# Kernel optimization log

Measured on AMD Instinct MI355X. Metric: run time of the kernel, lower is better.

Reference implementation:

```python
import jax, jax.numpy as jnp
import numpy as np

N_NODES = 100000
N_EDGES = 1600000


def _gcn_layer(feat, W, b, src, dst, n_nodes, pre_transform, activation):
    # GraphConv with norm='right': aggregate copy_src+sum, divide by in-degree (clamped to 1)
    if pre_transform:  # in_feats > out_feats: matmul first, then SpMM
        h = feat @ W
        agg = jax.ops.segment_sum(h[src], dst, num_segments=n_nodes)
    else:              # aggregate first, then matmul
        agg = jax.ops.segment_sum(feat[src], dst, num_segments=n_nodes)
        agg = agg @ W
    deg = jax.ops.segment_sum(jnp.ones((src.shape[0],), feat.dtype), dst, num_segments=n_nodes)
    rst = agg / jnp.clip(deg, 1.0)[:, None]
    rst = rst + b
    if activation:
        rst = jax.nn.relu(rst)
    return rst


def setup_inputs() -> dict:
    key = jax.random.key(0)
    ks = jax.random.split(key, 6)
    def xavier(k, shp):
        bound = float(np.sqrt(6.0 / (shp[0] + shp[1])))
        return jax.random.uniform(k, shp, jnp.float32, -bound, bound)
    return {
        "feat": jax.random.normal(ks[0], (N_NODES, 256), jnp.float32),
        "W0": xavier(ks[1], (256, 64)),
        "b0": jnp.zeros((64,), jnp.float32),
        "W1": xavier(ks[2], (64, 64)),
        "b1": jnp.zeros((64,), jnp.float32),
        "W2": xavier(ks[3], (64, 32)),
        "b2": jnp.zeros((32,), jnp.float32),
        "src": jax.random.randint(ks[4], (N_EDGES,), 0, N_NODES, jnp.int32),
        "dst": jax.random.randint(ks[5], (N_EDGES,), 0, N_NODES, jnp.int32),
    }


def reference(feat, W0, b0, W1, b1, W2, b2, src, dst):
    n = feat.shape[0]
    # layer 0: in 256 > out 64 -> pre-transform; relu
    h = _gcn_layer(feat, W0, b0, src, dst, n, pre_transform=True, activation=True)
    # layer 1: in 64 == out 64 -> aggregate then matmul; relu
    h = _gcn_layer(h, W1, b1, src, dst, n, pre_transform=False, activation=True)
    # layer 2: in 64 > out 32 -> pre-transform; no activation
    h = _gcn_layer(h, W2, b2, src, dst, n, pre_transform=True, activation=False)
    return h
```

## Files before the change

### kernel.cpp

```cpp
#include <hip/hip_runtime.h>
#include <hip/hip_bf16.h>
#include <hip/hip_fp16.h>


constexpr int NB_SHIFT = 7;
constexpr int EPB = 8192;
constexpr int MAXNB = 800;

using half8  = __attribute__((ext_vector_type(8))) _Float16;
using floatx4 = __attribute__((ext_vector_type(4))) float;

__global__ __launch_bounds__(256) void passA_hist(const int* __restrict__ dst, int* __restrict__ C_T,
                                                  int nb, int nblk, int n_edges) {
    __shared__ int h[MAXNB];
    for (int i = threadIdx.x; i < nb; i += 256) h[i] = 0;
    __syncthreads();
    const int e0 = blockIdx.x * EPB;
    const int e1 = min(e0 + EPB, n_edges);
    for (int i = e0 + threadIdx.x; i < e1; i += 256)
        atomicAdd(&h[dst[i] >> NB_SHIFT], 1);
    __syncthreads();
    for (int i = threadIdx.x; i < nb; i += 256)
        C_T[i * nblk + blockIdx.x] = h[i];
}

__global__ __launch_bounds__(256) void bucket_prefix(int* __restrict__ C_T, int* __restrict__ totals,
                                                     int nblk) {
    __shared__ int s[256];
    const int b = blockIdx.x, t = threadIdx.x;
    int v = (t < nblk) ? C_T[b * nblk + t] : 0;
    s[t] = v; __syncthreads();
    for (int off = 1; off < 256; off <<= 1) {
        int x = (t >= off) ? s[t - off] : 0;
        __syncthreads();
        s[t] += x;
        __syncthreads();
    }
    if (t < nblk) C_T[b * nblk + t] = s[t] - v;
    if (t == 255) totals[b] = s[255];
}

__global__ __launch_bounds__(256) void scan_base(const int* __restrict__ totals, int* __restrict__ base_out,
                                                 int* __restrict__ rowptr, int nb, int n, int n_edges) {
    __shared__ int s[256];
    const int t = threadIdx.x;
    int v[4]; int ts = 0;
#pragma unroll
    for (int j = 0; j < 4; ++j) { int i = t * 4 + j; v[j] = (i < nb) ? totals[i] : 0; ts += v[j]; }
    s[t] = ts; __syncthreads();
    for (int off = 1; off < 256; off <<= 1) {
        int x = (t >= off) ? s[t - off] : 0;
        __syncthreads();
        s[t] += x;
        __syncthreads();
    }
    int run = s[t] - ts;
#pragma unroll
    for (int j = 0; j < 4; ++j) { int i = t * 4 + j; if (i < nb) base_out[i] = run; run += v[j]; }
    if (t == 255) base_out[nb] = s[255];
    if (t == 0) rowptr[n] = n_edges;
}

__global__ __launch_bounds__(256) void passB_scatter(const int* __restrict__ src, const int* __restrict__ dst,
                                                     const int* __restrict__ C_T, const int* __restrict__ base,
                                                     int* __restrict__ sorted_pk, int nb, int nblk, int n_edges) {
    __shared__ int cur[MAXNB];
    const int blk = blockIdx.x;
    for (int i = threadIdx.x; i < nb; i += 256) cur[i] = base[i] + C_T[i * nblk + blk];
    __syncthreads();
    const int e0 = blk * EPB;
    const int e1 = min(e0 + EPB, n_edges);
    for (int i = e0 + threadIdx.x; i < e1; i += 256) {
        int d = dst[i];
        int p = atomicAdd(&cur[d >> NB_SHIFT], 1);
        sorted_pk[p] = ((d & 127) << 17) | src[i];
    }
}

__global__ __launch_bounds__(256) void passC_build(const int* __restrict__ sorted_pk, const int* __restrict__ base,
                                                   int* __restrict__ rowptr, int* __restrict__ col,
                                                   float* __restrict__ invd, int n) {
    __shared__ int degl[128];
    __shared__ int s[256];
    __shared__ int curl[128];
    const int b = blockIdx.x, t = threadIdx.x;
    const int node0 = b << NB_SHIFT;
    const int nn = min(128, n - node0);
    const int e0 = base[b], e1 = base[b + 1];
    if (t < 128) degl[t] = 0;
    __syncthreads();
    for (int i = e0 + t; i < e1; i += 256)
        atomicAdd(&degl[sorted_pk[i] >> 17], 1);
    __syncthreads();
    int d = (t < 128) ? degl[t] : 0;
    s[t] = d; __syncthreads();
    for (int off = 1; off < 128; off <<= 1) {
        int x = (t >= off) ? s[t - off] : 0;
        __syncthreads();
        s[t] += x;
        __syncthreads();
    }
    if (t < 128) {
        int excl = s[t] - d;
        curl[t] = excl;
        if (t < nn) {
            rowptr[node0 + t] = e0 + excl;
            invd[node0 + t] = 1.0f / (float)(d > 0 ? d : 1);
        }
    }
    __syncthreads();
    for (int i = e0 + t; i < e1; i += 256) {
        int pk = sorted_pk[i];
        int p = atomicAdd(&curl[pk >> 17], 1);
        col[e0 + p] = pk & 0x1FFFF;
    }
}

__device__ inline float4 load4(const float* p) { return *(const float4*)p; }
__device__ inline float4 load4(const __half* p) {
    __half2 a = *(const __half2*)p;
    __half2 b = *(const __half2*)(p + 2);
    float2 fa = __half22float2(a), fb = __half22float2(b);
    return make_float4(fa.x, fa.y, fb.x, fb.y);
}
__device__ inline void store4(float* p, float x0, float x1, float x2, float x3) {
    *(float4*)p = make_float4(x0, x1, x2, x3);
}
__device__ inline void store4(__half* p, float x0, float x1, float x2, float x3) {
    union { __half h[4]; int2 i2; } u;
    u.h[0] = __float2half(x0); u.h[1] = __float2half(x1);
    u.h[2] = __float2half(x2); u.h[3] = __float2half(x3);
    *(int2*)p = u.i2;
}

template <int FEATS, int EPI, typename OutT>
__global__ __launch_bounds__(256) void agg_kernel(const __half* __restrict__ X, const int* __restrict__ col,
                                                  const int* __restrict__ rowptr,
                                                  const float* __restrict__ inv_deg,
                                                  const float* __restrict__ bias,
                                                  OutT* __restrict__ out, int n) {
    constexpr int LPE = FEATS / 4;
    constexpr int EPW = 64 / LPE;
    const int node = blockIdx.x * 4 + (threadIdx.x >> 6);
    if (node >= n) return;
    const int lane = threadIdx.x & 63;
    const int eg = lane / LPE;
    const int fl = lane % LPE;
    const int s = rowptr[node], e = rowptr[node + 1];

    float ax = 0.f, ay = 0.f, az = 0.f, aw = 0.f;
    if (e > s) {
        int i = s + eg;
        const int nfull = (e - s) / EPW;
        int cc = col[min(i, e - 1)];
#pragma unroll 2
        for (int b = 0; b < nfull; ++b) {
            int cn = col[min(i + EPW, e - 1)];
            const __half* p = X + (size_t)cc * FEATS + fl * 4;
            float2 f01 = __half22float2(*(const __half2*)p);
            float2 f23 = __half22float2(*(const __half2*)(p + 2));
            ax += f01.x; ay += f01.y; az += f23.x; aw += f23.y;
            cc = cn; i += EPW;
        }
        if (i < e) {
            const __half* p = X + (size_t)cc * FEATS + fl * 4;
            float2 f01 = __half22float2(*(const __half2*)p);
            float2 f23 = __half22float2(*(const __half2*)(p + 2));
            ax += f01.x; ay += f01.y; az += f23.x; aw += f23.y;
        }
    }
#pragma unroll
    for (int m = LPE; m < 64; m <<= 1) {
        ax += __shfl_xor(ax, m);
        ay += __shfl_xor(ay, m);
        az += __shfl_xor(az, m);
        aw += __shfl_xor(aw, m);
    }
    if (eg == 0) {
        if (EPI != 0) {
            float sc = inv_deg[node];
            ax = ax * sc + bias[fl * 4 + 0];
            ay = ay * sc + bias[fl * 4 + 1];
            az = az * sc + bias[fl * 4 + 2];
            aw = aw * sc + bias[fl * 4 + 3];
            if (EPI == 1) {
                ax = fmaxf(ax, 0.f); ay = fmaxf(ay, 0.f);
                az = fmaxf(az, 0.f); aw = fmaxf(aw, 0.f);
            }
        }
        store4(&out[(size_t)node * FEATS + fl * 4], ax, ay, az, aw);
    }
}

__global__ __launch_bounds__(256) void cvtW0t(const float* __restrict__ W0, __half* __restrict__ W0t) {
    int o = blockIdx.x * 256 + threadIdx.x;
    int c = o >> 8, k = o & 255;
    W0t[o] = __float2half(W0[k * 64 + c]);
}

__global__ __launch_bounds__(256) void gemm0_mfma(const float* __restrict__ A, const __half* __restrict__ W0t,
                                                  __half* __restrict__ out, int nrows) {
    constexpr int LDH = 280;
    __shared__ _Float16 As[64][LDH];
    __shared__ _Float16 Bs[64][LDH];
    const int t = threadIdx.x;
    const int wave = t >> 6, lane = t & 63;
    const int row0 = blockIdx.x * 64;

#pragma unroll
    for (int l = 0; l < 16; ++l) {
        int fid = t + l * 256;
        int r = fid >> 6, c4 = fid & 63;
        int grow = row0 + r;
        int gr = grow < nrows ? grow : 0;
        float4 v = *(const float4*)&A[(size_t)gr * 256 + c4 * 4];
        _Float16* p = &As[r][c4 * 4];
        p[0] = (_Float16)v.x; p[1] = (_Float16)v.y;
        p[2] = (_Float16)v.z; p[3] = (_Float16)v.w;
    }
#pragma unroll
    for (int l = 0; l < 8; ++l) {
        int fid = t + l * 256;
        int r = fid >> 5, c8 = fid & 31;
        *(half8*)&Bs[r][c8 * 8] = *(const half8*)&W0t[r * 256 + c8 * 8];
    }
    __syncthreads();

    const int ar = wave * 16 + (lane & 15);
    const int kh = (lane >> 4) * 8;
    floatx4 acc0 = {0.f, 0.f, 0.f, 0.f}, acc1 = acc0, acc2 = acc0, acc3 = acc0;
#pragma unroll
    for (int ks = 0; ks < 8; ++ks) {
        const int k0 = ks * 32 + kh;
        half8 a = *(half8*)&As[ar][k0];
        half8 b0 = *(half8*)&Bs[ 0 + (lane & 15)][k0];
        half8 b1 = *(half8*)&Bs[16 + (lane & 15)][k0];
        half8 b2 = *(half8*)&Bs[32 + (lane & 15)][k0];
        half8 b3 = *(half8*)&Bs[48 + (lane & 15)][k0];
        acc0 = __builtin_amdgcn_mfma_f32_16x16x32_f16(a, b0, acc0, 0, 0, 0);
        acc1 = __builtin_amdgcn_mfma_f32_16x16x32_f16(a, b1, acc1, 0, 0, 0);
        acc2 = __builtin_amdgcn_mfma_f32_16x16x32_f16(a, b2, acc2, 0, 0, 0);
        acc3 = __builtin_amdgcn_mfma_f32_16x16x32_f16(a, b3, acc3, 0, 0, 0);
    }

    const int cc = lane & 15;
    const int rb = wave * 16 + (lane >> 4) * 4;
#pragma unroll
    for (int i = 0; i < 4; ++i) {
        int r = row0 + rb + i;
        if (r < nrows) {
            __half* po = &out[(size_t)r * 64];
            po[ 0 + cc] = __float2half(acc0[i]);
            po[16 + cc] = __float2half(acc1[i]);
            po[32 + cc] = __float2half(acc2[i]);
            po[48 + cc] = __float2half(acc3[i]);
        }
    }
}

__global__ __launch_bounds__(256) void gemm12_kernel(const __half* __restrict__ A2, const float* __restrict__ W1,
                                                     const float* __restrict__ b1, const float* __restrict__ W2,
                                                     const float* __restrict__ inv_deg,
                                                     __half* __restrict__ out, int nrows) {
    __shared__ float As[64][68];
    __shared__ float W1s[64][64];
    __shared__ float W2s[64][32];
    const int t = threadIdx.x;
    const int row0 = blockIdx.x * 64;
    const int cg = t % 16, rg = t / 16;

#pragma unroll
    for (int l = 0; l < 4; ++l) {
        int fid = t + l * 256;
        int r = fid / 16, c4 = fid % 16;
        int grow = row0 + r;
        int gr = grow < nrows ? grow : 0;
        float4 v = load4(&A2[(size_t)gr * 64 + c4 * 4]);
        *(float4*)&As[r][c4 * 4] = v;
    }
#pragma unroll
    for (int l = 0; l < 4; ++l) {
        int fid = t + l * 256;
        int r = fid / 16, c4 = fid % 16;
        *(float4*)&W1s[r][c4 * 4] = *(const float4*)&W1[(size_t)r * 64 + c4 * 4];
    }
#pragma unroll
    for (int l = 0; l < 2; ++l) {
        int fid = t + l * 256;
        int r = fid / 8, c4 = fid % 8;
        *(float4*)&W2s[r][c4 * 4] = *(const float4*)&W2[(size_t)r * 32 + c4 * 4];
    }
    __syncthreads();

    float acc[4][4] = {};
#pragma unroll 8
    for (int k = 0; k < 64; ++k) {
        float4 w = *(float4*)&W1s[k][cg * 4];
#pragma unroll
        for (int i = 0; i < 4; ++i) {
            float a = As[rg * 4 + i][k];
            acc[i][0] += a * w.x;
            acc[i][1] += a * w.y;
            acc[i][2] += a * w.z;
            acc[i][3] += a * w.w;
        }
    }
    __syncthreads();

#pragma unroll
    for (int i = 0; i < 4; ++i) {
        int r = row0 + rg * 4 + i;
        float sc = (r < nrows) ? inv_deg[r] : 0.f;
        float x0 = fmaxf(acc[i][0] * sc + b1[cg * 4 + 0], 0.f);
        float x1 = fmaxf(acc[i][1] * sc + b1[cg * 4 + 1], 0.f);
        float x2 = fmaxf(acc[i][2] * sc + b1[cg * 4 + 2], 0.f);
        float x3 = fmaxf(acc[i][3] * sc + b1[cg * 4 + 3], 0.f);
        *(float4*)&As[rg * 4 + i][cg * 4] = make_float4(x0, x1, x2, x3);
    }
    __syncthreads();

    const int cg2 = t % 8, rg2 = t / 8;
    float acc2[2][4] = {};
#pragma unroll 8
    for (int k = 0; k < 64; ++k) {
        float4 w = *(float4*)&W2s[k][cg2 * 4];
#pragma unroll
        for (int i = 0; i < 2; ++i) {
            float a = As[rg2 * 2 + i][k];
            acc2[i][0] += a * w.x;
            acc2[i][1] += a * w.y;
            acc2[i][2] += a * w.z;
            acc2[i][3] += a * w.w;
        }
    }
#pragma unroll
    for (int i = 0; i < 2; ++i) {
        int r = row0 + rg2 * 2 + i;
        if (r < nrows)
            store4(&out[(size_t)r * 32 + cg2 * 4], acc2[i][0], acc2[i][1], acc2[i][2], acc2[i][3]);
    }
}

extern "C" void kernel_launch(void* const* d_in, const int* in_sizes, int n_in,
                              void* d_out, int out_size, void* d_ws, size_t ws_size,
                              hipStream_t stream) {
    const float* feat = (const float*)d_in[0];
    const float* W0   = (const float*)d_in[1];
    const float* b0   = (const float*)d_in[2];
    const float* W1   = (const float*)d_in[3];
    const float* b1   = (const float*)d_in[4];
    const float* W2   = (const float*)d_in[5];
    const float* b2   = (const float*)d_in[6];
    const int*   src  = (const int*)d_in[7];
    const int*   dstv = (const int*)d_in[8];

    const int n = in_sizes[0] / 256;
    const int e = in_sizes[7];

    const int nb   = (n + 127) >> NB_SHIFT;
    const int nblk = (e + EPB - 1) / EPB;

    char* base_p = (char*)d_ws;
    size_t off = 0;
    auto alloc = [&](size_t bytes) -> char* {
        char* p = base_p + off;
        off += (bytes + 255) & ~(size_t)255;
        return p;
    };
    float*  invd   = (float*)alloc((size_t)n * 4);
    int*    rowptr = (int*)alloc((size_t)(n + 1) * 4);
    int*    bbase  = (int*)alloc((size_t)(MAXNB + 1) * 4);
    int*    totals = (int*)alloc((size_t)MAXNB * 4);
    __half* W0t    = (__half*)alloc((size_t)256 * 64 * 2);
    int*    col    = (int*)alloc((size_t)e * 4);
    __half* bufH1  = (__half*)alloc((size_t)n * 64 * 2);
    __half* bufH2  = (__half*)alloc((size_t)n * 64 * 2);
    (void)ws_size;

    int* C_T       = col;
    int* sorted_pk = (int*)bufH1;

    passA_hist   <<<nblk, 256, 0, stream>>>(dstv, C_T, nb, nblk, e);
    bucket_prefix<<<nb,   256, 0, stream>>>(C_T, totals, nblk);
    scan_base    <<<1,    256, 0, stream>>>(totals, bbase, rowptr, nb, n, e);
    passB_scatter<<<nblk, 256, 0, stream>>>(src, dstv, C_T, bbase, sorted_pk, nb, nblk, e);
    passC_build  <<<nb,   256, 0, stream>>>(sorted_pk, bbase, rowptr, col, invd, n);
    cvtW0t       <<<64,   256, 0, stream>>>(W0, W0t);

    const int gemm_blocks = (n + 63) / 64;
    const int agg_blocks  = (n + 3) / 4;

    gemm0_mfma<<<gemm_blocks, 256, 0, stream>>>(feat, W0t, bufH1, n);
    agg_kernel<64, 1, __half><<<agg_blocks, 256, 0, stream>>>(bufH1, col, rowptr, invd, b0, bufH2, n);

    agg_kernel<64, 0, __half><<<agg_blocks, 256, 0, stream>>>(bufH2, col, rowptr, nullptr, nullptr, bufH1, n);
    gemm12_kernel<<<gemm_blocks, 256, 0, stream>>>(bufH1, W1, b1, W2, invd, bufH2, n);

    agg_kernel<32, 2, float><<<agg_blocks, 256, 0, stream>>>(bufH2, col, rowptr, invd, b2, (float*)d_out, n);
}
```

Baseline: 214.8 us.

## Fuse layer-2 matmul into final aggregation and enlarge CSR-build buckets

Layer 2 now aggregates the 64-wide layer-1 output first and applies W2 inside the final aggregation kernel, instead of running the W2 matmul in the gemm kernel and aggregating a 32-wide result. This removes the second matmul stage from the gemm kernel but doubles the gather width of the last SpMM and adds a shared-memory matvec per node. The CSR-build buckets also grow from 128 to 512 nodes, with 512-thread passC blocks, cutting the bucket count and per-bucket overhead.

```diff
diff --git a/kernel.cpp b/kernel.cpp
--- a/kernel.cpp
+++ b/kernel.cpp
@@ -3,11 +3,11 @@
 #include <hip/hip_fp16.h>
 
 
-constexpr int NB_SHIFT = 7;
+constexpr int NB_SHIFT = 9;
 constexpr int EPB = 8192;
-constexpr int MAXNB = 800;
-
-using half8  = __attribute__((ext_vector_type(8))) _Float16;
+constexpr int MAXNB = 200;
+
+using half8   = __attribute__((ext_vector_type(8))) _Float16;
 using floatx4 = __attribute__((ext_vector_type(4))) float;
 
 __global__ __launch_bounds__(256) void passA_hist(const int* __restrict__ dst, int* __restrict__ C_T,
@@ -73,50 +73,47 @@
     for (int i = e0 + threadIdx.x; i < e1; i += 256) {
         int d = dst[i];
         int p = atomicAdd(&cur[d >> NB_SHIFT], 1);
-        sorted_pk[p] = ((d & 127) << 17) | src[i];
-    }
-}
-
-__global__ __launch_bounds__(256) void passC_build(const int* __restrict__ sorted_pk, const int* __restrict__ base,
+        sorted_pk[p] = ((d & 511) << 17) | src[i];
+    }
+}
+
+__global__ __launch_bounds__(512) void passC_build(const int* __restrict__ sorted_pk, const int* __restrict__ base,
                                                    int* __restrict__ rowptr, int* __restrict__ col,
                                                    float* __restrict__ invd, int n) {
-    __shared__ int degl[128];
-    __shared__ int s[256];
-    __shared__ int curl[128];
+    __shared__ int degl[512];
+    __shared__ int s[512];
+    __shared__ int curl[512];
     const int b = blockIdx.x, t = threadIdx.x;
     const int node0 = b << NB_SHIFT;
-    const int nn = min(128, n - node0);
+    const int nn = min(512, n - node0);
     const int e0 = base[b], e1 = base[b + 1];
-    if (t < 128) degl[t] = 0;
-    __syncthreads();
-    for (int i = e0 + t; i < e1; i += 256)
+    degl[t] = 0;
+    __syncthreads();
+    for (int i = e0 + t; i < e1; i += 512)
         atomicAdd(&degl[sorted_pk[i] >> 17], 1);
     __syncthreads();
-    int d = (t < 128) ? degl[t] : 0;
+    int d = degl[t];
     s[t] = d; __syncthreads();
-    for (int off = 1; off < 128; off <<= 1) {
+    for (int off = 1; off < 512; off <<= 1) {
         int x = (t >= off) ? s[t - off] : 0;
         __syncthreads();
         s[t] += x;
         __syncthreads();
     }
-    if (t < 128) {
-        int excl = s[t] - d;
-        curl[t] = excl;
-        if (t < nn) {
-            rowptr[node0 + t] = e0 + excl;
-            invd[node0 + t] = 1.0f / (float)(d > 0 ? d : 1);
-        }
-    }
-    __syncthreads();
-    for (int i = e0 + t; i < e1; i += 256) {
+    int excl = s[t] - d;
+    curl[t] = excl;
+    if (t < nn) {
+        rowptr[node0 + t] = e0 + excl;
+        invd[node0 + t] = 1.0f / (float)(d > 0 ? d : 1);
+    }
+    __syncthreads();
+    for (int i = e0 + t; i < e1; i += 512) {
         int pk = sorted_pk[i];
         int p = atomicAdd(&curl[pk >> 17], 1);
         col[e0 + p] = pk & 0x1FFFF;
     }
 }
 
-__device__ inline float4 load4(const float* p) { return *(const float4*)p; }
 __device__ inline float4 load4(const __half* p) {
     __half2 a = *(const __half2*)p;
     __half2 b = *(const __half2*)(p + 2);
@@ -133,14 +130,14 @@
     *(int2*)p = u.i2;
 }
 
-template <int FEATS, int EPI, typename OutT>
+template <int EPI>
 __global__ __launch_bounds__(256) void agg_kernel(const __half* __restrict__ X, const int* __restrict__ col,
                                                   const int* __restrict__ rowptr,
                                                   const float* __restrict__ inv_deg,
                                                   const float* __restrict__ bias,
-                                                  OutT* __restrict__ out, int n) {
-    constexpr int LPE = FEATS / 4;
-    constexpr int EPW = 64 / LPE;
+                                                  __half* __restrict__ out, int n) {
+    constexpr int LPE = 16;
+    constexpr int EPW = 4;
     const int node = blockIdx.x * 4 + (threadIdx.x >> 6);
     if (node >= n) return;
     const int lane = threadIdx.x & 63;
@@ -156,14 +153,14 @@
 #pragma unroll 2
         for (int b = 0; b < nfull; ++b) {
             int cn = col[min(i + EPW, e - 1)];
-            const __half* p = X + (size_t)cc * FEATS + fl * 4;
+            const __half* p = X + (size_t)cc * 64 + fl * 4;
             float2 f01 = __half22float2(*(const __half2*)p);
             float2 f23 = __half22float2(*(const __half2*)(p + 2));
             ax += f01.x; ay += f01.y; az += f23.x; aw += f23.y;
             cc = cn; i += EPW;
         }
         if (i < e) {
-            const __half* p = X + (size_t)cc * FEATS + fl * 4;
+            const __half* p = X + (size_t)cc * 64 + fl * 4;
             float2 f01 = __half22float2(*(const __half2*)p);
             float2 f23 = __half22float2(*(const __half2*)(p + 2));
             ax += f01.x; ay += f01.y; az += f23.x; aw += f23.y;
@@ -179,17 +176,78 @@
     if (eg == 0) {
         if (EPI != 0) {
             float sc = inv_deg[node];
-            ax = ax * sc + bias[fl * 4 + 0];
-            ay = ay * sc + bias[fl * 4 + 1];
-            az = az * sc + bias[fl * 4 + 2];
-            aw = aw * sc + bias[fl * 4 + 3];
-            if (EPI == 1) {
-                ax = fmaxf(ax, 0.f); ay = fmaxf(ay, 0.f);
-                az = fmaxf(az, 0.f); aw = fmaxf(aw, 0.f);
-            }
-        }
-        store4(&out[(size_t)node * FEATS + fl * 4], ax, ay, az, aw);
-    }
+            ax = fmaxf(ax * sc + bias[fl * 4 + 0], 0.f);
+            ay = fmaxf(ay * sc + bias[fl * 4 + 1], 0.f);
+            az = fmaxf(az * sc + bias[fl * 4 + 2], 0.f);
+            aw = fmaxf(aw * sc + bias[fl * 4 + 3], 0.f);
+        }
+        store4(&out[(size_t)node * 64 + fl * 4], ax, ay, az, aw);
+    }
+}
+
+__global__ __launch_bounds__(256) void agg_out_kernel(const __half* __restrict__ X2, const int* __restrict__ col,
+                                                      const int* __restrict__ rowptr,
+                                                      const float* __restrict__ inv_deg,
+                                                      const float* __restrict__ W2, const float* __restrict__ b2,
+                                                      float* __restrict__ out, int n) {
+    __shared__ float W2s[64][33];
+    __shared__ float vbuf[4][64];
+    const int t = threadIdx.x;
+#pragma unroll
+    for (int l = 0; l < 8; ++l) {
+        int o = t + l * 256;
+        W2s[o >> 5][o & 31] = W2[o];
+    }
+    __syncthreads();
+
+    const int node = blockIdx.x * 4 + (t >> 6);
+    if (node >= n) return;
+    const int wave = t >> 6, lane = t & 63;
+    const int eg = lane >> 4, fl = lane & 15;
+    const int s = rowptr[node], e = rowptr[node + 1];
+
+    float ax = 0.f, ay = 0.f, az = 0.f, aw = 0.f;
+    if (e > s) {
+        int i = s + eg;
+        const int nfull = (e - s) / 4;
+        int cc = col[min(i, e - 1)];
+#pragma unroll 2
+        for (int b = 0; b < nfull; ++b) {
+            int cn = col[min(i + 4, e - 1)];
+            const __half* p = X2 + (size_t)cc * 64 + fl * 4;
+            float2 f01 = __half22float2(*(const __half2*)p);
+            float2 f23 = __half22float2(*(const __half2*)(p + 2));
+            ax += f01.x; ay += f01.y; az += f23.x; aw += f23.y;
+            cc = cn; i += 4;
+        }
+        if (i < e) {
+            const __half* p = X2 + (size_t)cc * 64 + fl * 4;
+            float2 f01 = __half22float2(*(const __half2*)p);
+            float2 f23 = __half22float2(*(const __half2*)(p + 2));
+            ax += f01.x; ay += f01.y; az += f23.x; aw += f23.y;
+        }
+    }
+#pragma unroll
+    for (int m = 16; m < 64; m <<= 1) {
+        ax += __shfl_xor(ax, m);
+        ay += __shfl_xor(ay, m);
+        az += __shfl_xor(az, m);
+        aw += __shfl_xor(aw, m);
+    }
+    if (eg == 0) {
+        float sc = inv_deg[node];
+        vbuf[wave][fl * 4 + 0] = ax * sc;
+        vbuf[wave][fl * 4 + 1] = ay * sc;
+        vbuf[wave][fl * 4 + 2] = az * sc;
+        vbuf[wave][fl * 4 + 3] = aw * sc;
+    }
+    const int c = lane & 31, kh = (lane >> 5) * 32;
+    float sum = 0.f;
+#pragma unroll 8
+    for (int k = 0; k < 32; ++k)
+        sum += vbuf[wave][kh + k] * W2s[kh + k][c];
+    sum += __shfl_xor(sum, 32);
+    if (lane < 32) out[(size_t)node * 32 + c] = sum + b2[c];
 }
 
 __global__ __launch_bounds__(256) void cvtW0t(const float* __restrict__ W0, __half* __restrict__ W0t) {
@@ -258,13 +316,11 @@
     }
 }
 
-__global__ __launch_bounds__(256) void gemm12_kernel(const __half* __restrict__ A2, const float* __restrict__ W1,
-                                                     const float* __restrict__ b1, const float* __restrict__ W2,
-                                                     const float* __restrict__ inv_deg,
-                                                     __half* __restrict__ out, int nrows) {
+__global__ __launch_bounds__(256) void gemm1_kernel(const __half* __restrict__ A2, const float* __restrict__ W1,
+                                                    const float* __restrict__ b1, const float* __restrict__ inv_deg,
+                                                    __half* __restrict__ out, int nrows) {
     __shared__ float As[64][68];
     __shared__ float W1s[64][64];
-    __shared__ float W2s[64][32];
     const int t = threadIdx.x;
     const int row0 = blockIdx.x * 64;
     const int cg = t % 16, rg = t / 16;
@@ -284,12 +340,6 @@
         int r = fid / 16, c4 = fid % 16;
         *(float4*)&W1s[r][c4 * 4] = *(const float4*)&W1[(size_t)r * 64 + c4 * 4];
     }
-#pragma unroll
-    for (int l = 0; l < 2; ++l) {
-        int fid = t + l * 256;
-        int r = fid / 8, c4 = fid % 8;
-        *(float4*)&W2s[r][c4 * 4] = *(const float4*)&W2[(size_t)r * 32 + c4 * 4];
-    }
     __syncthreads();
 
     float acc[4][4] = {};
@@ -305,39 +355,18 @@
             acc[i][3] += a * w.w;
         }
     }
-    __syncthreads();
 
 #pragma unroll
     for (int i = 0; i < 4; ++i) {
         int r = row0 + rg * 4 + i;
-        float sc = (r < nrows) ? inv_deg[r] : 0.f;
-        float x0 = fmaxf(acc[i][0] * sc + b1[cg * 4 + 0], 0.f);
-        float x1 = fmaxf(acc[i][1] * sc + b1[cg * 4 + 1], 0.f);
-        float x2 = fmaxf(acc[i][2] * sc + b1[cg * 4 + 2], 0.f);
-        float x3 = fmaxf(acc[i][3] * sc + b1[cg * 4 + 3], 0.f);
-        *(float4*)&As[rg * 4 + i][cg * 4] = make_float4(x0, x1, x2, x3);
-    }
-    __syncthreads();
-
-    const int cg2 = t % 8, rg2 = t / 8;
-    float acc2[2][4] = {};
-#pragma unroll 8
-    for (int k = 0; k < 64; ++k) {
-        float4 w = *(float4*)&W2s[k][cg2 * 4];
-#pragma unroll
-        for (int i = 0; i < 2; ++i) {
-            float a = As[rg2 * 2 + i][k];
-            acc2[i][0] += a * w.x;
-            acc2[i][1] += a * w.y;
-            acc2[i][2] += a * w.z;
-            acc2[i][3] += a * w.w;
-        }
-    }
-#pragma unroll
-    for (int i = 0; i < 2; ++i) {
-        int r = row0 + rg2 * 2 + i;
-        if (r < nrows)
-            store4(&out[(size_t)r * 32 + cg2 * 4], acc2[i][0], acc2[i][1], acc2[i][2], acc2[i][3]);
+        if (r < nrows) {
+            float sc = inv_deg[r];
+            float x0 = fmaxf(acc[i][0] * sc + b1[cg * 4 + 0], 0.f);
+            float x1 = fmaxf(acc[i][1] * sc + b1[cg * 4 + 1], 0.f);
+            float x2 = fmaxf(acc[i][2] * sc + b1[cg * 4 + 2], 0.f);
+            float x3 = fmaxf(acc[i][3] * sc + b1[cg * 4 + 3], 0.f);
+            store4(&out[(size_t)r * 64 + cg * 4], x0, x1, x2, x3);
+        }
     }
 }
 
@@ -357,7 +386,7 @@
     const int n = in_sizes[0] / 256;
     const int e = in_sizes[7];
 
-    const int nb   = (n + 127) >> NB_SHIFT;
+    const int nb   = (n + 511) >> NB_SHIFT;
     const int nblk = (e + EPB - 1) / EPB;
 
     char* base_p = (char*)d_ws;
@@ -384,17 +413,17 @@
     bucket_prefix<<<nb,   256, 0, stream>>>(C_T, totals, nblk);
     scan_base    <<<1,    256, 0, stream>>>(totals, bbase, rowptr, nb, n, e);
     passB_scatter<<<nblk, 256, 0, stream>>>(src, dstv, C_T, bbase, sorted_pk, nb, nblk, e);
-    passC_build  <<<nb,   256, 0, stream>>>(sorted_pk, bbase, rowptr, col, invd, n);
+    passC_build  <<<nb,   512, 0, stream>>>(sorted_pk, bbase, rowptr, col, invd, n);
     cvtW0t       <<<64,   256, 0, stream>>>(W0, W0t);
 
     const int gemm_blocks = (n + 63) / 64;
     const int agg_blocks  = (n + 3) / 4;
 
     gemm0_mfma<<<gemm_blocks, 256, 0, stream>>>(feat, W0t, bufH1, n);
-    agg_kernel<64, 1, __half><<<agg_blocks, 256, 0, stream>>>(bufH1, col, rowptr, invd, b0, bufH2, n);
-
-    agg_kernel<64, 0, __half><<<agg_blocks, 256, 0, stream>>>(bufH2, col, rowptr, nullptr, nullptr, bufH1, n);
-    gemm12_kernel<<<gemm_blocks, 256, 0, stream>>>(bufH1, W1, b1, W2, invd, bufH2, n);
-
-    agg_kernel<32, 2, float><<<agg_blocks, 256, 0, stream>>>(bufH2, col, rowptr, invd, b2, (float*)d_out, n);
-}
+    agg_kernel<1><<<agg_blocks, 256, 0, stream>>>(bufH1, col, rowptr, invd, b0, bufH2, n);
+
+    agg_kernel<0><<<agg_blocks, 256, 0, stream>>>(bufH2, col, rowptr, nullptr, nullptr, bufH1, n);
+    gemm1_kernel<<<gemm_blocks, 256, 0, stream>>>(bufH1, W1, b1, invd, bufH2, n);
+
+    agg_out_kernel<<<agg_blocks, 256, 0, stream>>>(bufH2, col, rowptr, invd, W2, b2, (float*)d_out, n);
+}
```

Result: slower. 233.1 us (+8.5%).

## Port layer-1/2 GEMM to fp16 MFMA and shrink edge-block size

Applied to the files above, without the earlier changes.

Replaces the scalar fp32 fused W1/W2 GEMM with an MFMA 16x16x32 fp16 kernel that reads pre-transposed fp16 weights, which a merged weight-conversion kernel now produces. The intermediate ReLU output is kept in fp16 in shared memory. EPB is cut from 8192 to 2048 to give the histogram and scatter passes more blocks, and bucket_prefix now handles up to 1024 blocks per bucket. The fp16 intermediate loses some precision, and the smaller EPB produces a larger C_T table and more atomics traffic in the prefix stage.

```diff
diff --git a/kernel.cpp b/kernel.cpp
--- a/kernel.cpp
+++ b/kernel.cpp
@@ -4,10 +4,10 @@
 
 
 constexpr int NB_SHIFT = 7;
-constexpr int EPB = 8192;
+constexpr int EPB = 2048;
 constexpr int MAXNB = 800;
 
-using half8  = __attribute__((ext_vector_type(8))) _Float16;
+using half8   = __attribute__((ext_vector_type(8))) _Float16;
 using floatx4 = __attribute__((ext_vector_type(4))) float;
 
 __global__ __launch_bounds__(256) void passA_hist(const int* __restrict__ dst, int* __restrict__ C_T,
@@ -28,15 +28,19 @@
                                                      int nblk) {
     __shared__ int s[256];
     const int b = blockIdx.x, t = threadIdx.x;
-    int v = (t < nblk) ? C_T[b * nblk + t] : 0;
-    s[t] = v; __syncthreads();
+    int v[4]; int ts = 0;
+#pragma unroll
+    for (int j = 0; j < 4; ++j) { int i = t * 4 + j; v[j] = (i < nblk) ? C_T[b * nblk + i] : 0; ts += v[j]; }
+    s[t] = ts; __syncthreads();
     for (int off = 1; off < 256; off <<= 1) {
         int x = (t >= off) ? s[t - off] : 0;
         __syncthreads();
         s[t] += x;
         __syncthreads();
     }
-    if (t < nblk) C_T[b * nblk + t] = s[t] - v;
+    int run = s[t] - ts;
+#pragma unroll
+    for (int j = 0; j < 4; ++j) { int i = t * 4 + j; if (i < nblk) C_T[b * nblk + i] = run; run += v[j]; }
     if (t == 255) totals[b] = s[255];
 }
 
@@ -116,13 +120,6 @@
     }
 }
 
-__device__ inline float4 load4(const float* p) { return *(const float4*)p; }
-__device__ inline float4 load4(const __half* p) {
-    __half2 a = *(const __half2*)p;
-    __half2 b = *(const __half2*)(p + 2);
-    float2 fa = __half22float2(a), fb = __half22float2(b);
-    return make_float4(fa.x, fa.y, fb.x, fb.y);
-}
 __device__ inline void store4(float* p, float x0, float x1, float x2, float x3) {
     *(float4*)p = make_float4(x0, x1, x2, x3);
 }
@@ -192,10 +189,21 @@
     }
 }
 
-__global__ __launch_bounds__(256) void cvtW0t(const float* __restrict__ W0, __half* __restrict__ W0t) {
-    int o = blockIdx.x * 256 + threadIdx.x;
-    int c = o >> 8, k = o & 255;
-    W0t[o] = __float2half(W0[k * 64 + c]);
+__global__ __launch_bounds__(256) void cvt_weights(const float* __restrict__ W0, const float* __restrict__ W1,
+                                                   const float* __restrict__ W2,
+                                                   __half* __restrict__ W0t, __half* __restrict__ W1t,
+                                                   __half* __restrict__ W2t) {
+    const int b = blockIdx.x, t = threadIdx.x;
+    if (b < 64) {
+        int o = b * 256 + t;
+        W0t[o] = __float2half(W0[(o & 255) * 64 + (o >> 8)]);
+    } else if (b < 80) {
+        int o = (b - 64) * 256 + t;
+        W1t[o] = __float2half(W1[(o & 63) * 64 + (o >> 6)]);
+    } else {
+        int o = (b - 80) * 256 + t;
+        W2t[o] = __float2half(W2[(o & 63) * 32 + (o >> 6)]);
+    }
 }
 
 __global__ __launch_bounds__(256) void gemm0_mfma(const float* __restrict__ A, const __half* __restrict__ W0t,
@@ -258,86 +266,89 @@
     }
 }
 
-__global__ __launch_bounds__(256) void gemm12_kernel(const __half* __restrict__ A2, const float* __restrict__ W1,
-                                                     const float* __restrict__ b1, const float* __restrict__ W2,
-                                                     const float* __restrict__ inv_deg,
-                                                     __half* __restrict__ out, int nrows) {
-    __shared__ float As[64][68];
-    __shared__ float W1s[64][64];
-    __shared__ float W2s[64][32];
+__global__ __launch_bounds__(256) void gemm12_mfma(const __half* __restrict__ A2, const __half* __restrict__ W1t,
+                                                   const float* __restrict__ b1, const __half* __restrict__ W2t,
+                                                   const float* __restrict__ inv_deg,
+                                                   __half* __restrict__ out, int nrows) {
+    constexpr int LDH = 72;
+    __shared__ _Float16 As [64][LDH];
+    __shared__ _Float16 B1s[64][LDH];
+    __shared__ _Float16 B2s[32][LDH];
+    __shared__ _Float16 X2s[64][LDH];
     const int t = threadIdx.x;
+    const int wave = t >> 6, lane = t & 63;
     const int row0 = blockIdx.x * 64;
-    const int cg = t % 16, rg = t / 16;
-
-#pragma unroll
-    for (int l = 0; l < 4; ++l) {
+
+#pragma unroll
+    for (int l = 0; l < 2; ++l) {
         int fid = t + l * 256;
-        int r = fid / 16, c4 = fid % 16;
+        int r = fid >> 3, c8 = fid & 7;
         int grow = row0 + r;
         int gr = grow < nrows ? grow : 0;
-        float4 v = load4(&A2[(size_t)gr * 64 + c4 * 4]);
-        *(float4*)&As[r][c4 * 4] = v;
-    }
-#pragma unroll
-    for (int l = 0; l < 4; ++l) {
-        int fid = t + l * 256;
-        int r = fid / 16, c4 = fid % 16;
-        *(float4*)&W1s[r][c4 * 4] = *(const float4*)&W1[(size_t)r * 64 + c4 * 4];
+        *(half8*)&As[r][c8 * 8] = *(const half8*)&A2[(size_t)gr * 64 + c8 * 8];
     }
 #pragma unroll
     for (int l = 0; l < 2; ++l) {
         int fid = t + l * 256;
-        int r = fid / 8, c4 = fid % 8;
-        *(float4*)&W2s[r][c4 * 4] = *(const float4*)&W2[(size_t)r * 32 + c4 * 4];
-    }
-    __syncthreads();
-
-    float acc[4][4] = {};
-#pragma unroll 8
-    for (int k = 0; k < 64; ++k) {
-        float4 w = *(float4*)&W1s[k][cg * 4];
-#pragma unroll
-        for (int i = 0; i < 4; ++i) {
-            float a = As[rg * 4 + i][k];
-            acc[i][0] += a * w.x;
-            acc[i][1] += a * w.y;
-            acc[i][2] += a * w.z;
-            acc[i][3] += a * w.w;
-        }
-    }
-    __syncthreads();
+        int r = fid >> 3, c8 = fid & 7;
+        *(half8*)&B1s[r][c8 * 8] = *(const half8*)&W1t[r * 64 + c8 * 8];
+    }
+    {
+        int r = t >> 3, c8 = t & 7;
+        *(half8*)&B2s[r][c8 * 8] = *(const half8*)&W2t[r * 64 + c8 * 8];
+    }
+    __syncthreads();
+
+    const int ar = wave * 16 + (lane & 15);
+    const int kh = (lane >> 4) * 8;
+    const int cc = lane & 15;
+    const int rb = wave * 16 + (lane >> 4) * 4;
+
+    floatx4 acc0 = {0.f, 0.f, 0.f, 0.f}, acc1 = acc0, acc2 = acc0, acc3 = acc0;
+#pragma unroll
+    for (int ks = 0; ks < 2; ++ks) {
+        const int k0 = ks * 32 + kh;
+        half8 a = *(half8*)&As[ar][k0];
+        half8 b0 = *(half8*)&B1s[ 0 + (lane & 15)][k0];
+        half8 b1v = *(half8*)&B1s[16 + (lane & 15)][k0];
+        half8 b2v = *(half8*)&B1s[32 + (lane & 15)][k0];
+        half8 b3v = *(half8*)&B1s[48 + (lane & 15)][k0];
+        acc0 = __builtin_amdgcn_mfma_f32_16x16x32_f16(a, b0, acc0, 0, 0, 0);
+        acc1 = __builtin_amdgcn_mfma_f32_16x16x32_f16(a, b1v, acc1, 0, 0, 0);
+        acc2 = __builtin_amdgcn_mfma_f32_16x16x32_f16(a, b2v, acc2, 0, 0, 0);
+        acc3 = __builtin_amdgcn_mfma_f32_16x16x32_f16(a, b3v, acc3, 0, 0, 0);
+    }
 
 #pragma unroll
     for (int i = 0; i < 4; ++i) {
-        int r = row0 + rg * 4 + i;
+        int r = row0 + rb + i;
         float sc = (r < nrows) ? inv_deg[r] : 0.f;
-        float x0 = fmaxf(acc[i][0] * sc + b1[cg * 4 + 0], 0.f);
-        float x1 = fmaxf(acc[i][1] * sc + b1[cg * 4 + 1], 0.f);
-        float x2 = fmaxf(acc[i][2] * sc + b1[cg * 4 + 2], 0.f);
-        float x3 = fmaxf(acc[i][3] * sc + b1[cg * 4 + 3], 0.f);
-        *(float4*)&As[rg * 4 + i][cg * 4] = make_float4(x0, x1, x2, x3);
-    }
-    __syncthreads();
-
-    const int cg2 = t % 8, rg2 = t / 8;
-    float acc2[2][4] = {};
-#pragma unroll 8
-    for (int k = 0; k < 64; ++k) {
-        float4 w = *(float4*)&W2s[k][cg2 * 4];
-#pragma unroll
-        for (int i = 0; i < 2; ++i) {
-            float a = As[rg2 * 2 + i][k];
-            acc2[i][0] += a * w.x;
-            acc2[i][1] += a * w.y;
-            acc2[i][2] += a * w.z;
-            acc2[i][3] += a * w.w;
-        }
-    }
-#pragma unroll
-    for (int i = 0; i < 2; ++i) {
-        int r = row0 + rg2 * 2 + i;
-        if (r < nrows)
-            store4(&out[(size_t)r * 32 + cg2 * 4], acc2[i][0], acc2[i][1], acc2[i][2], acc2[i][3]);
+        X2s[rb + i][ 0 + cc] = (_Float16)fmaxf(acc0[i] * sc + b1[ 0 + cc], 0.f);
+        X2s[rb + i][16 + cc] = (_Float16)fmaxf(acc1[i] * sc + b1[16 + cc], 0.f);
+        X2s[rb + i][32 + cc] = (_Float16)fmaxf(acc2[i] * sc + b1[32 + cc], 0.f);
+        X2s[rb + i][48 + cc] = (_Float16)fmaxf(acc3[i] * sc + b1[48 + cc], 0.f);
+    }
+    __syncthreads();
+
+    floatx4 acc4 = {0.f, 0.f, 0.f, 0.f}, acc5 = acc4;
+#pragma unroll
+    for (int ks = 0; ks < 2; ++ks) {
+        const int k0 = ks * 32 + kh;
+        half8 a = *(half8*)&X2s[ar][k0];
+        half8 c0 = *(half8*)&B2s[ 0 + (lane & 15)][k0];
+        half8 c1 = *(half8*)&B2s[16 + (lane & 15)][k0];
+        acc4 = __builtin_amdgcn_mfma_f32_16x16x32_f16(a, c0, acc4, 0, 0, 0);
+        acc5 = __builtin_amdgcn_mfma_f32_16x16x32_f16(a, c1, acc5, 0, 0, 0);
+    }
+
+#pragma unroll
+    for (int i = 0; i < 4; ++i) {
+        int r = row0 + rb + i;
+        if (r < nrows) {
+            __half* po = &out[(size_t)r * 32];
+            po[ 0 + cc] = __float2half(acc4[i]);
+            po[16 + cc] = __float2half(acc5[i]);
+        }
     }
 }
 
@@ -372,6 +383,8 @@
     int*    bbase  = (int*)alloc((size_t)(MAXNB + 1) * 4);
     int*    totals = (int*)alloc((size_t)MAXNB * 4);
     __half* W0t    = (__half*)alloc((size_t)256 * 64 * 2);
+    __half* W1t    = (__half*)alloc((size_t)64 * 64 * 2);
+    __half* W2t    = (__half*)alloc((size_t)32 * 64 * 2);
     int*    col    = (int*)alloc((size_t)e * 4);
     __half* bufH1  = (__half*)alloc((size_t)n * 64 * 2);
     __half* bufH2  = (__half*)alloc((size_t)n * 64 * 2);
@@ -385,7 +398,7 @@
     scan_base    <<<1,    256, 0, stream>>>(totals, bbase, rowptr, nb, n, e);
     passB_scatter<<<nblk, 256, 0, stream>>>(src, dstv, C_T, bbase, sorted_pk, nb, nblk, e);
     passC_build  <<<nb,   256, 0, stream>>>(sorted_pk, bbase, rowptr, col, invd, n);
-    cvtW0t       <<<64,   256, 0, stream>>>(W0, W0t);
+    cvt_weights  <<<88,   256, 0, stream>>>(W0, W1, W2, W0t, W1t, W2t);
 
     const int gemm_blocks = (n + 63) / 64;
     const int agg_blocks  = (n + 3) / 4;
@@ -394,7 +407,7 @@
     agg_kernel<64, 1, __half><<<agg_blocks, 256, 0, stream>>>(bufH1, col, rowptr, invd, b0, bufH2, n);
 
     agg_kernel<64, 0, __half><<<agg_blocks, 256, 0, stream>>>(bufH2, col, rowptr, nullptr, nullptr, bufH1, n);
-    gemm12_kernel<<<gemm_blocks, 256, 0, stream>>>(bufH1, W1, b1, W2, invd, bufH2, n);
+    gemm12_mfma<<<gemm_blocks, 256, 0, stream>>>(bufH1, W1t, b1, W2t, invd, bufH2, n);
 
     agg_kernel<32, 2, float><<<agg_blocks, 256, 0, stream>>>(bufH2, col, rowptr, invd, b2, (float*)d_out, n);
 }
```

Result: faster. 203.8 us (-5.1%).
